# Optimization experiments

Hardware: AMD Instinct MI355X
Metric: run time of the kernel (lower is better)

Reference implementation:

```python
import jax, jax.numpy as jnp
import numpy as np

GROUP_SIZE = 64  # int4 precision
QMAX = 7.0       # symmetric int4 quant scale divisor


def setup_inputs() -> dict:
    key = jax.random.key(0)
    ks = jax.random.split(key, 8)
    B, S, C_in, C_out, R = 1, 4096, 3072, 3072, 32
    G = C_in // GROUP_SIZE
    x = jax.random.normal(ks[0], (B, S, C_in), dtype=jnp.float32)
    # unpacked int4 weight codes in [0,16); reference subtracts 8 -> signed int4 [-8,7]
    qweight = jax.random.randint(ks[1], (C_out, C_in), 0, 16, dtype=jnp.int32)
    # small positive per-group, per-out-channel weight scales
    wscales = jax.random.uniform(ks[2], (G, C_out), dtype=jnp.float32) * 0.01 + 0.001
    # positive smoothing factors bounded away from zero
    smooth_factor = jax.random.uniform(ks[3], (C_in,), dtype=jnp.float32) + 0.5
    proj_down = jax.random.normal(ks[4], (C_in, R), dtype=jnp.float32) * (1.0 / np.sqrt(C_in))
    proj_up = jax.random.normal(ks[5], (C_out, R), dtype=jnp.float32) * (1.0 / np.sqrt(R))
    bias = jax.random.normal(ks[6], (C_out,), dtype=jnp.float32) * 0.02
    return {
        "x": x,
        "qweight": qweight,
        "wscales": wscales,
        "smooth_factor": smooth_factor,
        "proj_down": proj_down,
        "proj_up": proj_up,
        "bias": bias,
    }


def reference(x, qweight, wscales, smooth_factor, proj_down, proj_up, bias):
    B, S, C = x.shape
    C_out = qweight.shape[0]
    M = B * S
    G = C // GROUP_SIZE

    # --- smoothing: x_hat = x / s (SVDQuant smoothing on activations) ---
    xs = x.reshape(M, C) / smooth_factor  # (M, C)

    # --- low-rank branch hidden state (fused with quantization in CUDA kernel) ---
    lora_act = jnp.einsum('mc,cr->mr', xs, proj_down)  # (M, R)

    # --- dynamic per-token, per-group int4 activation quantization ---
    xg = xs.reshape(M, G, GROUP_SIZE)
    amax = jnp.max(jnp.abs(xg), axis=-1, keepdims=True)          # (M, G, 1)
    ascale = amax / QMAX
    q = jnp.clip(jnp.round(xg / jnp.maximum(ascale, 1e-8)), -8.0, 7.0)
    x_dq = (q * ascale).reshape(M, C)                            # dequantized activations

    # --- weight dequantization: signed int4 codes * per-group/out-channel scales ---
    qw = qweight.astype(jnp.float32) - 8.0                       # (C_out, C) in [-8, 7]
    w_dq = (qw.reshape(C_out, G, GROUP_SIZE) * wscales.T[:, :, None]).reshape(C_out, C)

    # --- quantized GEMM + low-rank correction + bias ---
    out = jnp.einsum('mc,oc->mo', x_dq, w_dq)
    out = out + jnp.einsum('mr,or->mo', lora_act, proj_up) + bias
    return out.reshape(B, S, C_out)
```

## Files before the change

kernel.cpp:

```cpp
#include <hip/hip_runtime.h>
#include <stdint.h>

typedef unsigned short u16;

#define MTOK 4096
#define CIN  3072
#define COUT 3072
#define RANK 32
#define KT48 48
#define RS   3136
#define LKSPLIT 16
#define LKC (CIN/LKSPLIT)

#define LORA_BLK (MTOK/128*LKSPLIT)
#define WDQ_BLK COUT


typedef __attribute__((ext_vector_type(8))) short bf16x8;
typedef __attribute__((ext_vector_type(4))) float f32x4;

__device__ __forceinline__ u16 f2bf(float f) {
  union { float f; unsigned u; } v; v.f = f;
  unsigned r = v.u + 0x7FFFu + ((v.u >> 16) & 1u);
  return (u16)(r >> 16);
}

__device__ __forceinline__ void gload_lds16(const void* g, void* l) {
  __builtin_amdgcn_global_load_lds(
      (const __attribute__((address_space(1))) unsigned int*)g,
      (__attribute__((address_space(3))) unsigned int*)l, 16, 0, 0);
}

__device__ __forceinline__ float quant1(float xs, float ascale, float qd) {
  float q = rintf(xs / qd);
  q = fminf(fmaxf(q, -8.f), 7.f);
  return q * ascale;
}

__global__ __launch_bounds__(256) void prep_kernel(
    const float* __restrict__ x, const float* __restrict__ smooth,
    const int* __restrict__ qw, const float* __restrict__ wsc,
    const float* __restrict__ pd, const float* __restrict__ pu,
    u16* __restrict__ xdq, u16* __restrict__ wdq, u16* __restrict__ pu_bf,
    float* __restrict__ lp)
{
  const int b = blockIdx.x;
  const int t = threadIdx.x;

  if (b < LORA_BLK) {
    __shared__ __align__(16) u16 sA[128 * 64];
    __shared__ __align__(16) u16 sB[32 * 64];
    const int m0 = (b >> 4) * 128;
    const int kblk = b & 15;
    const int wave = t >> 6, lane = t & 63;
    const int lm = lane & 15, lkq = (lane >> 4) * 8;

    f32x4 acc[2][2];
    const f32x4 fz = {0.f, 0.f, 0.f, 0.f};
#pragma unroll
    for (int i = 0; i < 2; ++i)
#pragma unroll
      for (int j = 0; j < 2; ++j) acc[i][j] = fz;

    for (int kt = 0; kt < LKC / 64; ++kt) {
      const int k0 = kblk * LKC + kt * 64;
      const int col = (t & 15) * 4;
#pragma unroll
      for (int it = 0; it < 8; ++it) {
        const int row = it * 16 + (t >> 4);
        const float4 xv = *(const float4*)(x + (size_t)(m0 + row) * CIN + k0 + col);
        const float4 sv = *(const float4*)(smooth + k0 + col);
        const float xs0 = xv.x / sv.x, xs1 = xv.y / sv.y;
        const float xs2 = xv.z / sv.z, xs3 = xv.w / sv.w;
        ushort4 ov;
        ov.x = f2bf(xs0); ov.y = f2bf(xs1); ov.z = f2bf(xs2); ov.w = f2bf(xs3);
        *(ushort4*)&sA[row * 64 + col] = ov;
        float a = fmaxf(fmaxf(fabsf(xs0), fabsf(xs1)), fmaxf(fabsf(xs2), fabsf(xs3)));
#pragma unroll
        for (int off = 1; off < 16; off <<= 1) a = fmaxf(a, __shfl_xor(a, off));
        const float ascale = a / 7.0f;
        const float qd = fmaxf(ascale, 1e-8f);
        ushort4 oq;
        oq.x = f2bf(quant1(xs0, ascale, qd));
        oq.y = f2bf(quant1(xs1, ascale, qd));
        oq.z = f2bf(quant1(xs2, ascale, qd));
        oq.w = f2bf(quant1(xs3, ascale, qd));
        *(ushort4*)(xdq + (size_t)(m0 + row) * RS + k0 + col) = oq;
      }
#pragma unroll
      for (int i = 0; i < 8; ++i) {
        const int idx = i * 256 + t;
        const int k = idx >> 5, r = idx & 31;
        sB[r * 64 + k] = f2bf(pd[(size_t)(k0 + k) * RANK + r]);
      }
      __syncthreads();
#pragma unroll
      for (int kk = 0; kk < 2; ++kk) {
        const int ko = kk * 32 + lkq;
        bf16x8 af[2], bfr[2];
#pragma unroll
        for (int i = 0; i < 2; ++i)
          af[i] = *(const bf16x8*)&sA[(wave * 32 + i * 16 + lm) * 64 + ko];
#pragma unroll
        for (int j = 0; j < 2; ++j)
          bfr[j] = *(const bf16x8*)&sB[(j * 16 + lm) * 64 + ko];
#pragma unroll
        for (int i = 0; i < 2; ++i)
#pragma unroll
          for (int j = 0; j < 2; ++j)
            acc[i][j] = __builtin_amdgcn_mfma_f32_16x16x32_bf16(af[i], bfr[j], acc[i][j], 0, 0, 0);
      }
      __syncthreads();
    }
    float* lpk = lp + (size_t)kblk * MTOK * RANK;
#pragma unroll
    for (int i = 0; i < 2; ++i)
#pragma unroll
      for (int j = 0; j < 2; ++j) {
        const int col = j * 16 + lm;
        const int row0 = m0 + wave * 32 + i * 16 + (lane >> 4) * 4;
#pragma unroll
        for (int r = 0; r < 4; ++r)
          lpk[(size_t)(row0 + r) * RANK + col] = acc[i][j][r];
      }
  } else {
    const int o = b - LORA_BLK;
    const int4* qrow = (const int4*)(qw + (size_t)o * CIN);
    u16* orow = wdq + (size_t)o * RS;
#pragma unroll
    for (int p = 0; p < 3; ++p) {
      const int c4 = p * 256 + t;
      const int g = (c4 * 4) >> 6;
      const float ws = wsc[g * COUT + o];
      const int4 qv = qrow[c4];
      ushort4 ov;
      ov.x = f2bf((float)(qv.x - 8) * ws);
      ov.y = f2bf((float)(qv.y - 8) * ws);
      ov.z = f2bf((float)(qv.z - 8) * ws);
      ov.w = f2bf((float)(qv.w - 8) * ws);
      ((ushort4*)orow)[c4] = ov;
    }
    if (t < RANK) pu_bf[(size_t)o * RANK + t] = f2bf(pu[(size_t)o * RANK + t]);
  }
}

__global__ __launch_bounds__(256) void lora_fix_kernel(
    const float* __restrict__ lp, u16* __restrict__ lora_bf)
{
  const int idx = blockIdx.x * 256 + threadIdx.x;
  const int m = idx >> 5, c = idx & 31;
  float s = 0.f;
#pragma unroll
  for (int k = 0; k < LKSPLIT; ++k) s += lp[((size_t)k * MTOK + m) * RANK + c];
  lora_bf[(size_t)m * RANK + c] = f2bf(s);
}


__device__ __forceinline__ void stage_half(const u16* __restrict__ g, u16* lds_base,
                                           int kt, int half, int buf, int t) {
#pragma unroll
  for (int r = 0; r < 2; ++r) {
    const int ld = r * 512 + t;
    const int row = ld >> 3;
    const int d = ld & 7;
    const int c16 = d ^ (row & 7);
    gload_lds16(g + (size_t)(half * 128 + row) * RS + kt * 64 + c16 * 8,
                lds_base + buf * 16384 + half * 8192 + ld * 8);
  }
}

#define DSA(buf, mh) \
  _Pragma("unroll") for (int i = 0; i < 4; ++i) { \
    const int rl = wm * 64 + i * 16 + lm; \
    _Pragma("unroll") for (int kk = 0; kk < 2; ++kk) \
      af[i][kk] = *(const bf16x8*)&lds[(buf)*16384 + (mh)*8192 + rl * 64 + \
                    ((((kk << 2) | q4) ^ (rl & 7)) << 3)]; \
  }

#define DSB(buf, nh, BF) \
  _Pragma("unroll") for (int j = 0; j < 2; ++j) { \
    const int rl = wn * 32 + j * 16 + lm; \
    _Pragma("unroll") for (int kk = 0; kk < 2; ++kk) \
      BF[j][kk] = *(const bf16x8*)&lds[32768 + (buf)*16384 + (nh)*8192 + rl * 64 + \
                    ((((kk << 2) | q4) ^ (rl & 7)) << 3)]; \
  }

#define MFMA_Q(mh, nh, BF) \
  __builtin_amdgcn_s_setprio(1); \
  _Pragma("unroll") for (int i = 0; i < 4; ++i) \
  _Pragma("unroll") for (int j = 0; j < 2; ++j) \
  _Pragma("unroll") for (int kk = 0; kk < 2; ++kk) \
    acc[(mh)*4 + i][(nh)*2 + j] = __builtin_amdgcn_mfma_f32_16x16x32_bf16( \
        af[i][kk], BF[j][kk], acc[(mh)*4 + i][(nh)*2 + j], 0, 0, 0); \
  __builtin_amdgcn_s_setprio(0);

#define PH_OPEN() \
  __builtin_amdgcn_sched_barrier(0); \
  __builtin_amdgcn_s_barrier(); \
  asm volatile("s_waitcnt lgkmcnt(0)" ::: "memory"); \
  __builtin_amdgcn_sched_barrier(0)

#define PH_CLOSE() \
  __builtin_amdgcn_sched_barrier(0); \
  __builtin_amdgcn_s_barrier(); \
  __builtin_amdgcn_sched_barrier(0)

#define VM4() asm volatile("s_waitcnt vmcnt(4)" ::: "memory")
#define VM0() asm volatile("s_waitcnt vmcnt(0)" ::: "memory")

#define TILE8(cur, S0, S1, S2, S3, VMI) do { \
  DSA(cur, 0); DSB(cur, 0, bf0); S0; \
  PH_OPEN(); MFMA_Q(0, 0, bf0); PH_CLOSE(); \
  DSB(cur, 1, bf1); S1; \
  PH_OPEN(); MFMA_Q(0, 1, bf1); PH_CLOSE(); \
  DSA(cur, 1); S2; \
  PH_OPEN(); MFMA_Q(1, 1, bf1); PH_CLOSE(); \
  S3; \
  PH_OPEN(); MFMA_Q(1, 0, bf0); VMI; PH_CLOSE(); \
} while (0)

__global__ __launch_bounds__(512, 2) void gemm_kernel(
    const u16* __restrict__ xdq, const u16* __restrict__ wdq,
    const u16* __restrict__ pu_bf, const u16* __restrict__ lora_bf,
    const float* __restrict__ bias, float* __restrict__ out)
{
  __shared__ __align__(16) u16 lds[65536];

  const int t = threadIdx.x;
  const int wid = t >> 6, lane = t & 63;
  const int wm = wid >> 2, wn = wid & 3;
  const int lm = lane & 15, q4 = lane >> 4;

  const int wg = blockIdx.x;
  const int swz = (wg & 7) * 24 + (wg >> 3);
  const int by = swz / 12, bx = swz % 12;
  const int m0 = by * 256, n0 = bx * 256;

  const u16* Ag = xdq + (size_t)m0 * RS;
  const u16* Bg = wdq + (size_t)n0 * RS;
  u16* ldsB = lds + 32768;

  f32x4 acc[8][4];
  const f32x4 fz = {0.f, 0.f, 0.f, 0.f};
#pragma unroll
  for (int i = 0; i < 8; ++i)
#pragma unroll
    for (int j = 0; j < 4; ++j) acc[i][j] = fz;

  bf16x8 af[4][2], bf0[2][2], bf1[2][2];

  stage_half(Ag, lds,  0, 0, 0, t);
  stage_half(Bg, ldsB, 0, 0, 0, t);
  stage_half(Ag, lds,  0, 1, 0, t);
  stage_half(Bg, ldsB, 0, 1, 0, t);
  stage_half(Ag, lds,  1, 0, 1, t);
  stage_half(Bg, ldsB, 1, 1, 1, t);
  VM4();
  __builtin_amdgcn_s_barrier();
  __builtin_amdgcn_sched_barrier(0);

  for (int T = 0; T < 46; T += 2) {
    TILE8(0,
          stage_half(Ag, lds,  T + 1, 1, 1, t),
          stage_half(Bg, ldsB, T + 1, 0, 1, t),
          stage_half(Ag, lds,  T + 2, 0, 0, t),
          stage_half(Bg, ldsB, T + 2, 1, 0, t),
          VM4());
    TILE8(1,
          stage_half(Ag, lds,  T + 2, 1, 0, t),
          stage_half(Bg, ldsB, T + 2, 0, 0, t),
          stage_half(Ag, lds,  T + 3, 0, 1, t),
          stage_half(Bg, ldsB, T + 3, 1, 1, t),
          VM4());
  }
  TILE8(0,
        stage_half(Ag, lds,  47, 1, 1, t),
        stage_half(Bg, ldsB, 47, 0, 1, t),
        (void)0,
        (void)0,
        VM0());
  TILE8(1, (void)0, (void)0, (void)0, (void)0, (void)0);

  bf16x8 bl[4];
#pragma unroll
  for (int b = 0; b < 4; ++b) {
    const int bcol = n0 + (b >> 1) * 128 + wn * 32 + (b & 1) * 16 + lm;
    bl[b] = *(const bf16x8*)(pu_bf + (size_t)bcol * RANK + q4 * 8);
  }
#pragma unroll
  for (int a = 0; a < 8; ++a) {
    const int arow = m0 + (a >> 2) * 128 + wm * 64 + (a & 3) * 16 + lm;
    const bf16x8 al = *(const bf16x8*)(lora_bf + (size_t)arow * RANK + q4 * 8);
#pragma unroll
    for (int b = 0; b < 4; ++b)
      acc[a][b] = __builtin_amdgcn_mfma_f32_16x16x32_bf16(al, bl[b], acc[a][b], 0, 0, 0);
  }

#pragma unroll
  for (int b = 0; b < 4; ++b) {
    const int col = n0 + (b >> 1) * 128 + wn * 32 + (b & 1) * 16 + lm;
    const float bv = bias[col];
#pragma unroll
    for (int a = 0; a < 8; ++a) {
      const int row0 = m0 + (a >> 2) * 128 + wm * 64 + (a & 3) * 16 + q4 * 4;
#pragma unroll
      for (int r = 0; r < 4; ++r)
        out[(size_t)(row0 + r) * COUT + col] = acc[a][b][r] + bv;
    }
  }
}

extern "C" void kernel_launch(void* const* d_in, const int* in_sizes, int n_in,
                              void* d_out, int out_size, void* d_ws, size_t ws_size,
                              hipStream_t stream) {
  const float* x      = (const float*)d_in[0];
  const int*   qw     = (const int*)d_in[1];
  const float* wsc    = (const float*)d_in[2];
  const float* smooth = (const float*)d_in[3];
  const float* pd     = (const float*)d_in[4];
  const float* pu     = (const float*)d_in[5];
  const float* bias   = (const float*)d_in[6];
  float* out = (float*)d_out;

  u16* xdq     = (u16*)d_ws;
  u16* wdq     = xdq + (size_t)MTOK * RS;
  u16* pu_bf   = wdq + (size_t)COUT * RS;
  u16* lora_bf = pu_bf + (size_t)COUT * RANK;
  float* lp    = (float*)(lora_bf + (size_t)MTOK * RANK);

  prep_kernel<<<LORA_BLK + WDQ_BLK, 256, 0, stream>>>(
      x, smooth, qw, wsc, pd, pu, xdq, wdq, pu_bf, lp);
  lora_fix_kernel<<<MTOK * RANK / 256, 256, 0, stream>>>(lp, lora_bf);
  gemm_kernel<<<192, 512, 0, stream>>>(
      xdq, wdq, pu_bf, lora_bf, bias, out);
}
```

Measured before the change: 226.7 us.

## Split prep into separate kernels and deepen GEMM global-to-LDS prefetch

The fused prep kernel becomes three kernels: weight dequant, activation quantization, and the LoRA down-projection. The quant kernel runs on smaller 64-row tiles, and the LoRA kernel re-reads x to do its own smoothing, which adds extra global traffic. The GEMM prefetch is reordered so a whole K tile is staged two steps ahead, with the waitcnt relaxed from vmcnt(4) to vmcnt(8), allowing more loads in flight. This aims to improve load balance in prep and hide memory latency in the GEMM, at the cost of extra launches and a second pass over x.

Result: slower. 251.8 us (+11.1%).

```diff
diff --git a/kernel.cpp b/kernel.cpp
--- a/kernel.cpp
+++ b/kernel.cpp
@@ -12,9 +12,6 @@
 #define LKSPLIT 16
 #define LKC (CIN/LKSPLIT)
 
-#define LORA_BLK (MTOK/128*LKSPLIT)
-#define WDQ_BLK COUT
-
 
 typedef __attribute__((ext_vector_type(8))) short bf16x8;
 typedef __attribute__((ext_vector_type(4))) float f32x4;
@@ -37,111 +34,134 @@
   return q * ascale;
 }
 
-__global__ __launch_bounds__(256) void prep_kernel(
+
+__global__ __launch_bounds__(256) void wdq_kernel(
+    const int* __restrict__ qw, const float* __restrict__ wsc,
+    const float* __restrict__ pu, u16* __restrict__ wdq, u16* __restrict__ pu_bf)
+{
+  const int o = blockIdx.x;
+  const int t = threadIdx.x;
+  const int4* qrow = (const int4*)(qw + (size_t)o * CIN);
+  u16* orow = wdq + (size_t)o * RS;
+#pragma unroll
+  for (int p = 0; p < 3; ++p) {
+    const int c4 = p * 256 + t;
+    const int g = (c4 * 4) >> 6;
+    const float ws = wsc[g * COUT + o];
+    const int4 qv = qrow[c4];
+    ushort4 ov;
+    ov.x = f2bf((float)(qv.x - 8) * ws);
+    ov.y = f2bf((float)(qv.y - 8) * ws);
+    ov.z = f2bf((float)(qv.z - 8) * ws);
+    ov.w = f2bf((float)(qv.w - 8) * ws);
+    ((ushort4*)orow)[c4] = ov;
+  }
+  if (t < RANK) pu_bf[(size_t)o * RANK + t] = f2bf(pu[(size_t)o * RANK + t]);
+}
+
+__global__ __launch_bounds__(256) void quant_kernel(
     const float* __restrict__ x, const float* __restrict__ smooth,
-    const int* __restrict__ qw, const float* __restrict__ wsc,
-    const float* __restrict__ pd, const float* __restrict__ pu,
-    u16* __restrict__ xdq, u16* __restrict__ wdq, u16* __restrict__ pu_bf,
-    float* __restrict__ lp)
+    u16* __restrict__ xdq)
 {
   const int b = blockIdx.x;
   const int t = threadIdx.x;
-
-  if (b < LORA_BLK) {
-    __shared__ __align__(16) u16 sA[128 * 64];
-    __shared__ __align__(16) u16 sB[32 * 64];
-    const int m0 = (b >> 4) * 128;
-    const int kblk = b & 15;
-    const int wave = t >> 6, lane = t & 63;
-    const int lm = lane & 15, lkq = (lane >> 4) * 8;
-
-    f32x4 acc[2][2];
-    const f32x4 fz = {0.f, 0.f, 0.f, 0.f};
-#pragma unroll
-    for (int i = 0; i < 2; ++i)
-#pragma unroll
-      for (int j = 0; j < 2; ++j) acc[i][j] = fz;
-
-    for (int kt = 0; kt < LKC / 64; ++kt) {
-      const int k0 = kblk * LKC + kt * 64;
-      const int col = (t & 15) * 4;
-#pragma unroll
-      for (int it = 0; it < 8; ++it) {
-        const int row = it * 16 + (t >> 4);
-        const float4 xv = *(const float4*)(x + (size_t)(m0 + row) * CIN + k0 + col);
-        const float4 sv = *(const float4*)(smooth + k0 + col);
-        const float xs0 = xv.x / sv.x, xs1 = xv.y / sv.y;
-        const float xs2 = xv.z / sv.z, xs3 = xv.w / sv.w;
-        ushort4 ov;
-        ov.x = f2bf(xs0); ov.y = f2bf(xs1); ov.z = f2bf(xs2); ov.w = f2bf(xs3);
-        *(ushort4*)&sA[row * 64 + col] = ov;
-        float a = fmaxf(fmaxf(fabsf(xs0), fabsf(xs1)), fmaxf(fabsf(xs2), fabsf(xs3)));
-#pragma unroll
-        for (int off = 1; off < 16; off <<= 1) a = fmaxf(a, __shfl_xor(a, off));
-        const float ascale = a / 7.0f;
-        const float qd = fmaxf(ascale, 1e-8f);
-        ushort4 oq;
-        oq.x = f2bf(quant1(xs0, ascale, qd));
-        oq.y = f2bf(quant1(xs1, ascale, qd));
-        oq.z = f2bf(quant1(xs2, ascale, qd));
-        oq.w = f2bf(quant1(xs3, ascale, qd));
-        *(ushort4*)(xdq + (size_t)(m0 + row) * RS + k0 + col) = oq;
-      }
-#pragma unroll
-      for (int i = 0; i < 8; ++i) {
-        const int idx = i * 256 + t;
-        const int k = idx >> 5, r = idx & 31;
-        sB[r * 64 + k] = f2bf(pd[(size_t)(k0 + k) * RANK + r]);
-      }
-      __syncthreads();
-#pragma unroll
-      for (int kk = 0; kk < 2; ++kk) {
-        const int ko = kk * 32 + lkq;
-        bf16x8 af[2], bfr[2];
-#pragma unroll
-        for (int i = 0; i < 2; ++i)
-          af[i] = *(const bf16x8*)&sA[(wave * 32 + i * 16 + lm) * 64 + ko];
+  const int m0 = (b >> 4) * 64;
+  const int kblk = b & 15;
+  const int col = (t & 15) * 4;
+#pragma unroll
+  for (int kt = 0; kt < 3; ++kt) {
+    const int k0 = kblk * LKC + kt * 64;
+#pragma unroll
+    for (int it = 0; it < 4; ++it) {
+      const int row = m0 + it * 16 + (t >> 4);
+      const float4 xv = *(const float4*)(x + (size_t)row * CIN + k0 + col);
+      const float4 sv = *(const float4*)(smooth + k0 + col);
+      const float xs0 = xv.x / sv.x, xs1 = xv.y / sv.y;
+      const float xs2 = xv.z / sv.z, xs3 = xv.w / sv.w;
+      float a = fmaxf(fmaxf(fabsf(xs0), fabsf(xs1)), fmaxf(fabsf(xs2), fabsf(xs3)));
+#pragma unroll
+      for (int off = 1; off < 16; off <<= 1) a = fmaxf(a, __shfl_xor(a, off));
+      const float ascale = a / 7.0f;
+      const float qd = fmaxf(ascale, 1e-8f);
+      ushort4 oq;
+      oq.x = f2bf(quant1(xs0, ascale, qd));
+      oq.y = f2bf(quant1(xs1, ascale, qd));
+      oq.z = f2bf(quant1(xs2, ascale, qd));
+      oq.w = f2bf(quant1(xs3, ascale, qd));
+      *(ushort4*)(xdq + (size_t)row * RS + k0 + col) = oq;
+    }
+  }
+}
+
+__global__ __launch_bounds__(256) void lora_kernel(
+    const float* __restrict__ x, const float* __restrict__ smooth,
+    const float* __restrict__ pd, float* __restrict__ lp)
+{
+  __shared__ __align__(16) u16 sA[128 * 64];
+  __shared__ __align__(16) u16 sB[32 * 64];
+  const int b = blockIdx.x;
+  const int t = threadIdx.x;
+  const int m0 = (b >> 4) * 128;
+  const int kblk = b & 15;
+  const int wave = t >> 6, lane = t & 63;
+  const int lm = lane & 15, lkq = (lane >> 4) * 8;
+
+  f32x4 acc[2][2];
+  const f32x4 fz = {0.f, 0.f, 0.f, 0.f};
+#pragma unroll
+  for (int i = 0; i < 2; ++i)
+#pragma unroll
+    for (int j = 0; j < 2; ++j) acc[i][j] = fz;
+
+  for (int kt = 0; kt < LKC / 64; ++kt) {
+    const int k0 = kblk * LKC + kt * 64;
+    const int col = (t & 15) * 4;
+#pragma unroll
+    for (int it = 0; it < 8; ++it) {
+      const int row = it * 16 + (t >> 4);
+      const float4 xv = *(const float4*)(x + (size_t)(m0 + row) * CIN + k0 + col);
+      const float4 sv = *(const float4*)(smooth + k0 + col);
+      ushort4 ov;
+      ov.x = f2bf(xv.x / sv.x); ov.y = f2bf(xv.y / sv.y);
+      ov.z = f2bf(xv.z / sv.z); ov.w = f2bf(xv.w / sv.w);
+      *(ushort4*)&sA[row * 64 + col] = ov;
+    }
+#pragma unroll
+    for (int i = 0; i < 8; ++i) {
+      const int idx = i * 256 + t;
+      const int k = idx >> 5, r = idx & 31;
+      sB[r * 64 + k] = f2bf(pd[(size_t)(k0 + k) * RANK + r]);
+    }
+    __syncthreads();
+#pragma unroll
+    for (int kk = 0; kk < 2; ++kk) {
+      const int ko = kk * 32 + lkq;
+      bf16x8 af[2], bfr[2];
+#pragma unroll
+      for (int i = 0; i < 2; ++i)
+        af[i] = *(const bf16x8*)&sA[(wave * 32 + i * 16 + lm) * 64 + ko];
+#pragma unroll
+      for (int j = 0; j < 2; ++j)
+        bfr[j] = *(const bf16x8*)&sB[(j * 16 + lm) * 64 + ko];
+#pragma unroll
+      for (int i = 0; i < 2; ++i)
 #pragma unroll
         for (int j = 0; j < 2; ++j)
-          bfr[j] = *(const bf16x8*)&sB[(j * 16 + lm) * 64 + ko];
-#pragma unroll
-        for (int i = 0; i < 2; ++i)
-#pragma unroll
-          for (int j = 0; j < 2; ++j)
-            acc[i][j] = __builtin_amdgcn_mfma_f32_16x16x32_bf16(af[i], bfr[j], acc[i][j], 0, 0, 0);
-      }
-      __syncthreads();
-    }
-    float* lpk = lp + (size_t)kblk * MTOK * RANK;
-#pragma unroll
-    for (int i = 0; i < 2; ++i)
-#pragma unroll
-      for (int j = 0; j < 2; ++j) {
-        const int col = j * 16 + lm;
-        const int row0 = m0 + wave * 32 + i * 16 + (lane >> 4) * 4;
-#pragma unroll
-        for (int r = 0; r < 4; ++r)
-          lpk[(size_t)(row0 + r) * RANK + col] = acc[i][j][r];
-      }
-  } else {
-    const int o = b - LORA_BLK;
-    const int4* qrow = (const int4*)(qw + (size_t)o * CIN);
-    u16* orow = wdq + (size_t)o * RS;
-#pragma unroll
-    for (int p = 0; p < 3; ++p) {
-      const int c4 = p * 256 + t;
-      const int g = (c4 * 4) >> 6;
-      const float ws = wsc[g * COUT + o];
-      const int4 qv = qrow[c4];
-      ushort4 ov;
-      ov.x = f2bf((float)(qv.x - 8) * ws);
-      ov.y = f2bf((float)(qv.y - 8) * ws);
-      ov.z = f2bf((float)(qv.z - 8) * ws);
-      ov.w = f2bf((float)(qv.w - 8) * ws);
-      ((ushort4*)orow)[c4] = ov;
-    }
-    if (t < RANK) pu_bf[(size_t)o * RANK + t] = f2bf(pu[(size_t)o * RANK + t]);
-  }
+          acc[i][j] = __builtin_amdgcn_mfma_f32_16x16x32_bf16(af[i], bfr[j], acc[i][j], 0, 0, 0);
+    }
+    __syncthreads();
+  }
+  float* lpk = lp + (size_t)kblk * MTOK * RANK;
+#pragma unroll
+  for (int i = 0; i < 2; ++i)
+#pragma unroll
+    for (int j = 0; j < 2; ++j) {
+      const int col = j * 16 + lm;
+      const int row0 = m0 + wave * 32 + i * 16 + (lane >> 4) * 4;
+#pragma unroll
+      for (int r = 0; r < 4; ++r)
+        lpk[(size_t)(row0 + r) * RANK + col] = acc[i][j][r];
+    }
 }
 
 __global__ __launch_bounds__(256) void lora_fix_kernel(
@@ -205,17 +225,17 @@
   __builtin_amdgcn_s_barrier(); \
   __builtin_amdgcn_sched_barrier(0)
 
-#define VM4() asm volatile("s_waitcnt vmcnt(4)" ::: "memory")
+#define VM8() asm volatile("s_waitcnt vmcnt(8)" ::: "memory")
 #define VM0() asm volatile("s_waitcnt vmcnt(0)" ::: "memory")
 
-#define TILE8(cur, S0, S1, S2, S3, VMI) do { \
-  DSA(cur, 0); DSB(cur, 0, bf0); S0; \
+#define TILE8(cur, S_A0, S_B0, S_B1, S_A1, VMI) do { \
+  DSA(cur, 0); DSB(cur, 0, bf0); \
   PH_OPEN(); MFMA_Q(0, 0, bf0); PH_CLOSE(); \
-  DSB(cur, 1, bf1); S1; \
+  DSB(cur, 1, bf1); S_A0; S_B0; \
   PH_OPEN(); MFMA_Q(0, 1, bf1); PH_CLOSE(); \
-  DSA(cur, 1); S2; \
+  DSA(cur, 1); S_B1; \
   PH_OPEN(); MFMA_Q(1, 1, bf1); PH_CLOSE(); \
-  S3; \
+  S_A1; \
   PH_OPEN(); MFMA_Q(1, 0, bf0); VMI; PH_CLOSE(); \
 } while (0)
 
@@ -251,34 +271,31 @@
 
   stage_half(Ag, lds,  0, 0, 0, t);
   stage_half(Bg, ldsB, 0, 0, 0, t);
+  stage_half(Bg, ldsB, 0, 1, 0, t);
   stage_half(Ag, lds,  0, 1, 0, t);
-  stage_half(Bg, ldsB, 0, 1, 0, t);
   stage_half(Ag, lds,  1, 0, 1, t);
+  stage_half(Bg, ldsB, 1, 0, 1, t);
   stage_half(Bg, ldsB, 1, 1, 1, t);
-  VM4();
+  stage_half(Ag, lds,  1, 1, 1, t);
+  VM8();
   __builtin_amdgcn_s_barrier();
   __builtin_amdgcn_sched_barrier(0);
 
   for (int T = 0; T < 46; T += 2) {
     TILE8(0,
-          stage_half(Ag, lds,  T + 1, 1, 1, t),
-          stage_half(Bg, ldsB, T + 1, 0, 1, t),
           stage_half(Ag, lds,  T + 2, 0, 0, t),
+          stage_half(Bg, ldsB, T + 2, 0, 0, t),
           stage_half(Bg, ldsB, T + 2, 1, 0, t),
-          VM4());
+          stage_half(Ag, lds,  T + 2, 1, 0, t),
+          VM8());
     TILE8(1,
-          stage_half(Ag, lds,  T + 2, 1, 0, t),
-          stage_half(Bg, ldsB, T + 2, 0, 0, t),
           stage_half(Ag, lds,  T + 3, 0, 1, t),
+          stage_half(Bg, ldsB, T + 3, 0, 1, t),
           stage_half(Bg, ldsB, T + 3, 1, 1, t),
-          VM4());
-  }
-  TILE8(0,
-        stage_half(Ag, lds,  47, 1, 1, t),
-        stage_half(Bg, ldsB, 47, 0, 1, t),
-        (void)0,
-        (void)0,
-        VM0());
+          stage_half(Ag, lds,  T + 3, 1, 1, t),
+          VM8());
+  }
+  TILE8(0, (void)0, (void)0, (void)0, (void)0, VM0());
   TILE8(1, (void)0, (void)0, (void)0, (void)0, (void)0);
 
   bf16x8 bl[4];
@@ -328,8 +345,9 @@
   u16* lora_bf = pu_bf + (size_t)COUT * RANK;
   float* lp    = (float*)(lora_bf + (size_t)MTOK * RANK);
 
-  prep_kernel<<<LORA_BLK + WDQ_BLK, 256, 0, stream>>>(
-      x, smooth, qw, wsc, pd, pu, xdq, wdq, pu_bf, lp);
+  wdq_kernel<<<COUT, 256, 0, stream>>>(qw, wsc, pu, wdq, pu_bf);
+  quant_kernel<<<1024, 256, 0, stream>>>(x, smooth, xdq);
+  lora_kernel<<<512, 256, 0, stream>>>(x, smooth, pd, lp);
   lora_fix_kernel<<<MTOK * RANK / 256, 256, 0, stream>>>(lp, lora_bf);
   gemm_kernel<<<192, 512, 0, stream>>>(
       xdq, wdq, pu_bf, lora_bf, bias, out);
```
